# Performance work log

Measured on AMD Instinct MI355X. Metric: run time of the kernel, lower is better.

The kernel has to match this reference:

```python
import jax, jax.numpy as jnp
import numpy as np

B, N1, N2, K, D, C_IN = 2, 8192, 8192, 16, 64, 131
MLP = [128, 128]
WN_HID = [8, 8]


def _sqdist(src, dst):
    # src [B,N,3], dst [B,M,3] -> [B,N,M], clamped at 0 like the torch code
    d = (jnp.sum(src * src, -1)[:, :, None]
         + jnp.sum(dst * dst, -1)[:, None, :]
         - 2.0 * jnp.einsum('bnc,bmc->bnm', src, dst))
    return jnp.maximum(d, 0.0)


def _knn(k, xyz, query):
    # k smallest distances (torch.topk largest=False)
    _, idx = jax.lax.top_k(-_sqdist(query, xyz), k)
    return idx  # [B,S,k]


def _gather(points, idx):
    # points [B,N,C], idx [B,S,K] -> [B,S,K,C]
    return jax.vmap(lambda p, i: p[i])(points, idx)


def _mlp(x, Ws, bs, act):
    # x [B,N,K,Cin]; 1x1 Conv2d == per-point linear
    for W, b in zip(Ws, bs):
        x = act(jnp.einsum('bnkc,oc->bnko', x, W) + b)
    return x


_leaky = lambda x: jax.nn.leaky_relu(x, 0.1)
_relu = jax.nn.relu


def setup_inputs() -> dict:
    key = jax.random.key(0)
    ks = iter(jax.random.split(key, 32))

    def conv(cout, cin):
        s = 1.0 / np.sqrt(cin)
        w = jax.random.uniform(next(ks), (cout, cin), jnp.float32, -s, s)
        b = jax.random.uniform(next(ks), (cout,), jnp.float32, -s, s)
        return w, b

    inp = {
        'pc1': jax.random.normal(next(ks), (B, 3, N1), jnp.float32),
        'pc2': jax.random.normal(next(ks), (B, 3, N2), jnp.float32),
        'feature1': jax.random.normal(next(ks), (B, D, N1), jnp.float32),
        'feature2': jax.random.normal(next(ks), (B, D, N2), jnp.float32),
    }
    # main mlp convs: 131 -> 128 -> 128
    c = C_IN
    for i, co in enumerate(MLP):
        inp[f'mlp_W{i}'], inp[f'mlp_b{i}'] = conv(co, c)
        c = co
    # weightnet1/2: 3 -> 8 -> 8 -> 128
    for name in ('wn1', 'wn2'):
        dims = [3] + WN_HID + [MLP[-1]]
        for i in range(len(dims) - 1):
            inp[f'{name}_W{i}'], inp[f'{name}_b{i}'] = conv(dims[i + 1], dims[i])
    return inp


def reference(pc1, pc2, feature1, feature2,
              mlp_W0, mlp_b0, mlp_W1, mlp_b1,
              wn1_W0, wn1_b0, wn1_W1, wn1_b1, wn1_W2, wn1_b2,
              wn2_W0, wn2_b0, wn2_W1, wn2_b1, wn2_W2, wn2_b2):
    nsample = K
    p1 = pc1.transpose(0, 2, 1)    # [B,N1,3]
    p2 = pc2.transpose(0, 2, 1)    # [B,N2,3]
    f1 = feature1.transpose(0, 2, 1)  # [B,N1,D1]
    f2 = feature2.transpose(0, 2, 1)  # [B,N2,D2]
    b, n1, _ = p1.shape

    # cross-cloud KNN grouping
    idx = _knn(nsample, p2, p1)                 # [B,N1,K]
    direction_xyz = _gather(p2, idx) - p1[:, :, None, :]   # [B,N1,K,3]
    gf2 = _gather(f2, idx)                      # [B,N1,K,D2]
    gf1 = jnp.broadcast_to(f1[:, :, None, :], (b, n1, nsample, f1.shape[-1]))
    new_features = jnp.concatenate([gf1, gf2, direction_xyz], -1)  # [B,N1,K,131]

    new_features = _mlp(new_features, [mlp_W0, mlp_W1], [mlp_b0, mlp_b1], _leaky)
    weights = _mlp(direction_xyz, [wn1_W0, wn1_W1, wn1_W2],
                   [wn1_b0, wn1_b1, wn1_b2], _relu)
    new_features = jnp.sum(weights * new_features, axis=2)  # [B,N1,Cout]

    # self KNN re-aggregation
    idx2 = _knn(nsample, p1, p1)
    dir2 = _gather(p1, idx2) - p1[:, :, None, :]
    weights2 = _mlp(dir2, [wn2_W0, wn2_W1, wn2_W2],
                    [wn2_b0, wn2_b1, wn2_b2], _relu)
    grouped = _gather(new_features, idx2)        # [B,N1,K,Cout]
    out = jnp.sum(weights2 * grouped, axis=2)    # [B,N1,Cout]
    return out.transpose(0, 2, 1)                # [B,Cout,N1]
```

## Files before the change

kernel.cpp:

```cpp
#include <hip/hip_runtime.h>

typedef __attribute__((ext_vector_type(8))) short short8;
typedef __attribute__((ext_vector_type(4))) float f32x4;

#define NPTS 8192
#define NB 2
#define KNN 16
#define KP 20
#define CAP 128
#define LDX 168
#define LDH 136

__device__ inline ushort f2bf(float x){
  unsigned u = __float_as_uint(x);
  return (ushort)((u + 0x7FFFu + ((u >> 16) & 1u)) >> 16);
}
__device__ inline float leaky(float x){ return x > 0.f ? x : 0.1f * x; }
__device__ inline f32x4 mfma16(short8 a, short8 b, f32x4 c){
  return __builtin_amdgcn_mfma_f32_16x16x32_bf16(a, b, c, 0, 0, 0);
}
__device__ inline int cellkey(float x, float y, float z){
  int ix = (int)((x + 3.f) * (16.f / 6.f));
  int iy = (int)((y + 3.f) * (16.f / 6.f));
  int iz = (int)((z + 3.f) * (16.f / 6.f));
  ix = ix < 0 ? 0 : (ix > 15 ? 15 : ix);
  iy = iy < 0 ? 0 : (iy > 15 ? 15 : iy);
  iz = iz < 0 ? 0 : (iz > 15 ? 15 : iz);
  int key = 0;
  #pragma unroll
  for (int i = 0; i < 4; ++i)
    key |= (((ix >> i) & 1) << (3 * i + 2)) | (((iy >> i) & 1) << (3 * i + 1)) | (((iz >> i) & 1) << (3 * i));
  return key;
}

__global__ __launch_bounds__(256) void k_misc(const float* __restrict__ pc1, const float* __restrict__ pc2,
                                              float4* __restrict__ p1, float4* __restrict__ p2,
                                              const float* __restrict__ W0, const float* __restrict__ W1,
                                              ushort* __restrict__ W0p, ushort* __restrict__ W1p){
  int bid = blockIdx.x;
  if (bid < 64){
    int i = bid * 256 + threadIdx.x;
    int b = i >> 13, n = i & (NPTS - 1);
    const float* s1 = pc1 + (size_t)b * 3 * NPTS + n;
    const float* s2 = pc2 + (size_t)b * 3 * NPTS + n;
    p1[i] = make_float4(s1[0], s1[NPTS], s1[2 * NPTS], 0.f);
    p2[i] = make_float4(s2[0], s2[NPTS], s2[2 * NPTS], 0.f);
  } else if (bid == 64){
    for (int e = threadIdx.x; e < 8 * 5 * 64 * 8; e += 256){
      int i = e & 7, ln = (e >> 3) & 63, t = e >> 9, kt = t % 5, ct = t / 5;
      int col = ct * 16 + (ln & 15), k = kt * 32 + 8 * (ln >> 4) + i;
      W0p[e] = f2bf(k < 131 ? W0[col * 131 + k] : 0.f);
    }
  } else {
    for (int e = threadIdx.x; e < 8 * 4 * 64 * 8; e += 256){
      int i = e & 7, ln = (e >> 3) & 63, t = e >> 9, kt = t & 3, ct = t >> 2;
      int col = ct * 16 + (ln & 15), k = kt * 32 + 8 * (ln >> 4) + i;
      W1p[e] = f2bf(W1[col * 128 + k]);
    }
  }
}

__global__ __launch_bounds__(256) void k_transpose(const float* __restrict__ f1, const float* __restrict__ f2,
                                                   ushort* __restrict__ o1, ushort* __restrict__ o2){
  __shared__ ushort tile[64][257];
  int bid = blockIdx.x;
  int feat = bid >> 6; int b = (bid >> 5) & 1; int n0 = (bid & 31) * 256;
  const float* src = (feat ? f2 : f1) + (size_t)b * 64 * NPTS;
  ushort* dst = (feat ? o2 : o1) + (size_t)b * NPTS * 64;
  for (int rep = 0; rep < 64; ++rep){
    int lin = rep * 256 + threadIdx.x;
    int j = lin >> 8, nn = lin & 255;
    tile[j][nn] = f2bf(src[(size_t)j * NPTS + n0 + nn]);
  }
  __syncthreads();
  for (int rep = 0; rep < 64; ++rep){
    int lin = rep * 256 + threadIdx.x;
    int nn = lin >> 6, j = lin & 63;
    dst[(size_t)(n0 + nn) * 64 + j] = tile[j][nn];
  }
}

__global__ __launch_bounds__(1024) void k_sort(const float4* __restrict__ p1, const float4* __restrict__ p2,
                                               float4* __restrict__ sp1, float4* __restrict__ sp2,
                                               int* __restrict__ cs1, int* __restrict__ cs2){
  __shared__ int hist[4096];
  __shared__ int tsum[1024];
  int bid = blockIdx.x;
  int b = bid >> 1, cloud = bid & 1;
  const float4* src = (cloud ? p2 : p1) + b * NPTS;
  float4* dst = (cloud ? sp2 : sp1) + b * NPTS;
  int* cs = (cloud ? cs2 : cs1) + b * 4100;
  int tid = threadIdx.x;
  #pragma unroll
  for (int i = 0; i < 4; ++i) hist[tid + i * 1024] = 0;
  __syncthreads();
  int keys[8];
  #pragma unroll
  for (int i = 0; i < 8; ++i){
    float4 v = src[i * 1024 + tid];
    keys[i] = cellkey(v.x, v.y, v.z);
    atomicAdd(&hist[keys[i]], 1);
  }
  __syncthreads();
  int h[4], s = 0;
  #pragma unroll
  for (int i = 0; i < 4; ++i){ h[i] = hist[tid * 4 + i]; s += h[i]; }
  tsum[tid] = s;
  __syncthreads();
  for (int off = 1; off < 1024; off <<= 1){
    int v = tsum[tid];
    if (tid >= off) v += tsum[tid - off];
    __syncthreads();
    tsum[tid] = v;
    __syncthreads();
  }
  int ex = tid ? tsum[tid - 1] : 0;
  #pragma unroll
  for (int i = 0; i < 4; ++i){ int c = h[i]; hist[tid * 4 + i] = ex; cs[tid * 4 + i] = ex; ex += c; }
  if (tid == 1023) cs[4096] = NPTS;
  __syncthreads();
  #pragma unroll
  for (int i = 0; i < 8; ++i){
    float4 v = src[i * 1024 + tid];
    int pos = atomicAdd(&hist[keys[i]], 1);
    dst[pos] = make_float4(v.x, v.y, v.z, __int_as_float(i * 1024 + tid));
  }
}

__global__ __launch_bounds__(256) void k_knn(const float4* __restrict__ p1,
                                             const float4* __restrict__ sp1, const float4* __restrict__ sp2,
                                             const int* __restrict__ cs1, const int* __restrict__ cs2,
                                             int* __restrict__ idx1, int* __restrict__ idx2){
  __shared__ float sx[1024], sy[1024], sz[1024];
  __shared__ int bufS[4][4][CAP];
  int tid = threadIdx.x, lane = tid & 63, wv = tid >> 6;
  int bid = blockIdx.x;
  int task = bid >> 10, rem = bid & 1023;
  int b = rem >> 9; int q0 = (rem & 511) * 16;
  const float4* __restrict__ cpb = (task ? sp1 : sp2) + b * NPTS;
  const int* __restrict__ cs = (task ? cs1 : cs2) + b * 4100;
  int* __restrict__ outIdx = task ? idx2 : idx1;
  int qbase = b * NPTS + q0 + wv * 4;
  float qx[4], qy[4], qz[4], thr[4]; int cnt[4];
  #pragma unroll
  for (int i = 0; i < 4; ++i){
    float4 qq = p1[qbase + i];
    qx[i] = qq.x; qy[i] = qq.y; qz[i] = qq.z;
  }
  #pragma unroll
  for (int q = 0; q < 4; ++q){
    int key = cellkey(qx[q], qy[q], qz[q]);
    int st = cs[key], en = cs[key + 1];
    int wstart = st + ((en - st) >> 1) - 128;
    wstart = wstart < 0 ? 0 : (wstart > NPTS - 256 ? NPTS - 256 : wstart);
    float dw[4];
    #pragma unroll
    for (int i = 0; i < 4; ++i){
      float4 c = cpb[wstart + i * 64 + lane];
      float dx = c.x - qx[q], dy = c.y - qy[q], dz = c.z - qz[q];
      dw[i] = fmaf(dx, dx, fmaf(dy, dy, dz * dz));
    }
    float mn = fminf(fminf(dw[0], dw[1]), fminf(dw[2], dw[3]));
    float mx = mn;
    #pragma unroll
    for (int off = 1; off < 64; off <<= 1) mx = fmaxf(mx, __shfl_xor(mx, off));
    float lo = 0.f, hi = __uint_as_float(__float_as_uint(mx) + 1u);
    #pragma unroll
    for (int it = 0; it < 16; ++it){
      float mid = 0.5f * (lo + hi);
      int c = __popcll(__ballot(dw[0] < mid)) + __popcll(__ballot(dw[1] < mid))
            + __popcll(__ballot(dw[2] < mid)) + __popcll(__ballot(dw[3] < mid));
      if (c >= KP) hi = mid; else lo = mid;
    }
    thr[q] = __uint_as_float(__float_as_uint(hi) + 1u);
    cnt[q] = 0;
  }
  for (int ch = 0; ch < 8; ++ch){
    __syncthreads();
    for (int t = tid; t < 1024; t += 256){
      float4 cc = cpb[ch * 1024 + t];
      sx[t] = cc.x; sy[t] = cc.y; sz[t] = cc.z;
    }
    __syncthreads();
    for (int it = 0; it < 16; ++it){
      float cx = sx[it * 64 + lane], cy = sy[it * 64 + lane], cz = sz[it * 64 + lane];
      int jb = ch * 1024 + it * 64;
      #pragma unroll
      for (int q = 0; q < 4; ++q){
        float dx = cx - qx[q], dy = cy - qy[q], dz = cz - qz[q];
        float d = fmaf(dx, dx, fmaf(dy, dy, dz * dz));
        bool pass = d < thr[q];
        unsigned long long m = __ballot(pass);
        if (m){
          int pre = __popcll(m & ((1ull << lane) - 1ull));
          int pos = cnt[q] + pre;
          if (pass && pos < CAP) bufS[wv][q][pos] = jb + lane;
          cnt[q] += __popcll(m);
        }
      }
    }
  }
  #pragma unroll 1
  for (int q = 0; q < 4; ++q){
    size_t orow = (size_t)(b * NPTS + q0 + wv * 4 + q) * KNN;
    int T = cnt[q];
    if (T <= CAP){
      double d0 = 1e300, d1 = 1e300; int o0 = 0, o1 = 0, s0 = 0x7fffffff, s1 = 0x7fffffff;
      if (lane < T){
        s0 = bufS[wv][q][lane];
        float4 c = cpb[s0];
        o0 = __float_as_int(c.w);
        double dx = (double)c.x - (double)qx[q];
        double dy = (double)c.y - (double)qy[q];
        double dz = (double)c.z - (double)qz[q];
        d0 = dx * dx + dy * dy + dz * dz;
      }
      if (lane + 64 < T){
        s1 = bufS[wv][q][lane + 64];
        float4 c = cpb[s1];
        o1 = __float_as_int(c.w);
        double dx = (double)c.x - (double)qx[q];
        double dy = (double)c.y - (double)qy[q];
        double dz = (double)c.z - (double)qz[q];
        d1 = dx * dx + dy * dy + dz * dz;
      }
      int r0 = 0, r1 = 0;
      #pragma unroll 4
      for (int j = 0; j < T; ++j){
        int sj = bufS[wv][q][j];
        float4 c = cpb[sj];
        double dx = (double)c.x - (double)qx[q];
        double dy = (double)c.y - (double)qy[q];
        double dz = (double)c.z - (double)qz[q];
        double dj = dx * dx + dy * dy + dz * dz;
        if (dj < d0 || (dj == d0 && sj < s0)) ++r0;
        if (dj < d1 || (dj == d1 && sj < s1)) ++r1;
      }
      if (lane < T && r0 < KNN) outIdx[orow + r0] = o0;
      if (lane + 64 < T && r1 < KNN) outIdx[orow + r1] = o1;
    } else {
      float sdq = 1e30f; int siq = 0; float th = thr[q];
      for (int t = lane; t < NPTS; t += 64){
        int base0 = t - lane;
        float4 c = cpb[t];
        float dx = c.x - qx[q], dy = c.y - qy[q], dz = c.z - qz[q];
        float d = fmaf(dx, dx, fmaf(dy, dy, dz * dz));
        unsigned long long m = __ballot(d < th);
        while (m){
          int src = __ffsll((unsigned long long)m) - 1;
          m &= m - 1;
          float dv = __shfl(d, src);
          if (dv >= th) continue;
          int iv = base0 + src;
          float ud = __shfl_up(sdq, 1);
          int   ui = __shfl_up(siq, 1);
          int pos = __popcll(__ballot(sdq <= dv) & 0xFFFFFull);
          bool lt = lane < pos;
          bool eq = lane == pos;
          float nd = lt ? sdq : (eq ? dv : ud);
          int   ni = lt ? siq : (eq ? iv : ui);
          sdq = nd; siq = ni;
          th = fminf(th, __shfl(nd, KP - 1));
        }
      }
      double dd = -1.0; int orig = 0;
      if (lane < KP){
        float4 cc = cpb[siq];
        orig = __float_as_int(cc.w);
        double dx = (double)cc.x - (double)qx[q];
        double dy = (double)cc.y - (double)qy[q];
        double dz = (double)cc.z - (double)qz[q];
        dd = dx * dx + dy * dy + dz * dz;
      }
      #pragma unroll
      for (int rep = 0; rep < 4; ++rep){
        double mx = dd; int mi = lane;
        #pragma unroll
        for (int off = 32; off; off >>= 1){
          double om = __shfl_xor(mx, off);
          int oi = __shfl_xor(mi, off);
          if (om > mx || (om == mx && oi < mi)){ mx = om; mi = oi; }
        }
        if (lane == mi) dd = -1.0;
      }
      unsigned long long keep = __ballot(dd >= 0.0);
      int rank = __popcll(keep & ((1ull << lane) - 1ull));
      if (dd >= 0.0) outIdx[orow + rank] = orig;
    }
  }
}

__global__ __launch_bounds__(256) void k_fused(
    const float4* __restrict__ p1, const float4* __restrict__ p2,
    const ushort* __restrict__ f1b, const ushort* __restrict__ f2b,
    const int* __restrict__ idx1,
    const ushort* __restrict__ W0p, const ushort* __restrict__ W1p,
    const float* __restrict__ b0, const float* __restrict__ b1,
    const float* __restrict__ wn1W0, const float* __restrict__ wn1b0,
    const float* __restrict__ wn1W1, const float* __restrict__ wn1b1,
    const float* __restrict__ wn1W2, const float* __restrict__ wn1b2,
    float* __restrict__ NF)
{
  __shared__ ushort Xs[128 * LDX];
  __shared__ float dirS[128][4];
  __shared__ float h2S[128][8];
  __shared__ float W2s[128][8];
  __shared__ float b0S[128], b1S[128], b2S[128];
  __shared__ int idxS[128];
  int tid = threadIdx.x, lane = tid & 63, wv = tid >> 6;
  int bid = blockIdx.x;
  int b = bid >> 10; int n0 = (bid & 1023) << 3;
  int base = b * NPTS;
  for (int t = tid; t < 1024; t += 256) ((float*)W2s)[t] = wn1W2[t];
  if (tid < 128){
    b0S[tid] = b0[tid]; b1S[tid] = b1[tid]; b2S[tid] = wn1b2[tid];
    int p = tid >> 4;
    int id = idx1[(size_t)(base + n0 + p) * KNN + (tid & 15)];
    idxS[tid] = id;
    float4 c = p2[base + id];
    float4 q = p1[base + n0 + p];
    float dx = c.x - q.x, dy = c.y - q.y, dz = c.z - q.z;
    dirS[tid][0] = dx; dirS[tid][1] = dy; dirS[tid][2] = dz; dirS[tid][3] = 0.f;
    ushort* xr = Xs + tid * LDX;
    xr[128] = f2bf(dx); xr[129] = f2bf(dy); xr[130] = f2bf(dz);
    #pragma unroll
    for (int j = 131; j < 160; ++j) xr[j] = 0;
  }
  __syncthreads();
  {
    int r = tid >> 1, hf = tid & 1;
    const uint4* s = (const uint4*)(hf ? (f2b + (size_t)(base + idxS[r]) * 64)
                                       : (f1b + (size_t)(base + n0 + (r >> 4)) * 64));
    uint4* d = (uint4*)(Xs + r * LDX + hf * 64);
    #pragma unroll
    for (int j = 0; j < 8; ++j) d[j] = s[j];
  }
  __syncthreads();
  int r0 = wv * 32;
  f32x4 zero4 = {0.f, 0.f, 0.f, 0.f};
  f32x4 acc[2][8];
  #pragma unroll
  for (int mt = 0; mt < 2; ++mt)
    #pragma unroll
    for (int ct = 0; ct < 8; ++ct) acc[mt][ct] = zero4;
  #pragma unroll
  for (int kt = 0; kt < 5; ++kt){
    const ushort* ab = Xs + (r0 + (lane & 15)) * LDX + kt * 32 + 8 * (lane >> 4);
    short8 a0 = *(const short8*)ab;
    short8 a1 = *(const short8*)(ab + 16 * LDX);
    #pragma unroll
    for (int ct = 0; ct < 8; ++ct){
      short8 bb = *(const short8*)(W0p + (size_t)((ct * 5 + kt) * 64 + lane) * 8);
      acc[0][ct] = mfma16(a0, bb, acc[0][ct]);
      acc[1][ct] = mfma16(a1, bb, acc[1][ct]);
    }
  }
  __syncthreads();
  ushort* Hs = Xs;
  #pragma unroll
  for (int mt = 0; mt < 2; ++mt)
    #pragma unroll
    for (int ct = 0; ct < 8; ++ct){
      int col = ct * 16 + (lane & 15);
      float bb = b0S[col];
      #pragma unroll
      for (int r = 0; r < 4; ++r){
        int row = r0 + mt * 16 + 4 * (lane >> 4) + r;
        Hs[row * LDH + col] = f2bf(leaky(acc[mt][ct][r] + bb));
      }
    }
  if (tid < 128){
    float d0 = dirS[tid][0], d1 = dirS[tid][1], d2 = dirS[tid][2];
    float h1[8];
    #pragma unroll
    for (int i = 0; i < 8; ++i)
      h1[i] = fmaxf(fmaf(wn1W0[i * 3 + 2], d2, fmaf(wn1W0[i * 3 + 1], d1, fmaf(wn1W0[i * 3], d0, wn1b0[i]))), 0.f);
    #pragma unroll
    for (int i = 0; i < 8; ++i){
      float s = wn1b1[i];
      #pragma unroll
      for (int j = 0; j < 8; ++j) s = fmaf(wn1W1[i * 8 + j], h1[j], s);
      h2S[tid][i] = fmaxf(s, 0.f);
    }
  }
  __syncthreads();
  #pragma unroll
  for (int mt = 0; mt < 2; ++mt)
    #pragma unroll
    for (int ct = 0; ct < 8; ++ct) acc[mt][ct] = zero4;
  #pragma unroll
  for (int kt = 0; kt < 4; ++kt){
    const ushort* ab = Hs + (r0 + (lane & 15)) * LDH + kt * 32 + 8 * (lane >> 4);
    short8 a0 = *(const short8*)ab;
    short8 a1 = *(const short8*)(ab + 16 * LDH);
    #pragma unroll
    for (int ct = 0; ct < 8; ++ct){
      short8 bb = *(const short8*)(W1p + (size_t)((ct * 4 + kt) * 64 + lane) * 8);
      acc[0][ct] = mfma16(a0, bb, acc[0][ct]);
      acc[1][ct] = mfma16(a1, bb, acc[1][ct]);
    }
  }
  #pragma unroll
  for (int ct = 0; ct < 8; ++ct){
    int col = ct * 16 + (lane & 15);
    float4 w2a = *(const float4*)&W2s[col][0];
    float4 w2b = *(const float4*)&W2s[col][4];
    float bw = b2S[col], bg = b1S[col];
    #pragma unroll
    for (int mt = 0; mt < 2; ++mt){
      float s = 0.f;
      #pragma unroll
      for (int r = 0; r < 4; ++r){
        int row = r0 + mt * 16 + 4 * (lane >> 4) + r;
        const float4 ha = *(const float4*)&h2S[row][0];
        const float4 hb = *(const float4*)&h2S[row][4];
        float w = bw;
        w = fmaf(w2a.x, ha.x, w); w = fmaf(w2a.y, ha.y, w); w = fmaf(w2a.z, ha.z, w); w = fmaf(w2a.w, ha.w, w);
        w = fmaf(w2b.x, hb.x, w); w = fmaf(w2b.y, hb.y, w); w = fmaf(w2b.z, hb.z, w); w = fmaf(w2b.w, hb.w, w);
        w = fmaxf(w, 0.f);
        float g = leaky(acc[mt][ct][r] + bg);
        s = fmaf(w, g, s);
      }
      s += __shfl_xor(s, 16);
      s += __shfl_xor(s, 32);
      if (lane < 16) NF[(size_t)(base + n0 + wv * 2 + mt) * 128 + col] = s;
    }
  }
}

__global__ __launch_bounds__(256) void k_reagg(
    const float4* __restrict__ p1, const int* __restrict__ idx2,
    const float* __restrict__ NF,
    const float* __restrict__ wn2W0, const float* __restrict__ wn2b0,
    const float* __restrict__ wn2W1, const float* __restrict__ wn2b1,
    const float* __restrict__ wn2W2, const float* __restrict__ wn2b2,
    float* __restrict__ out)
{
  __shared__ float h2L[4][16][8];
  __shared__ int idxL[4][16];
  __shared__ float outT[128][20];
  int tid = threadIdx.x, lane = tid & 63, wv = tid >> 6;
  int bid = blockIdx.x;
  int b = bid >> 9; int n0 = (bid & 511) * 16;
  int base = b * NPTS;
  for (int pp = 0; pp < 4; ++pp){
    int np = wv * 4 + pp;
    int n = n0 + np;
    if (lane < 16){
      int id = idx2[(size_t)(base + n) * KNN + lane];
      idxL[wv][lane] = id;
      float4 c = p1[base + id];
      float4 q = p1[base + n];
      float d0 = c.x - q.x, d1 = c.y - q.y, d2 = c.z - q.z;
      float h1[8];
      #pragma unroll
      for (int i = 0; i < 8; ++i)
        h1[i] = fmaxf(fmaf(wn2W0[i * 3 + 2], d2, fmaf(wn2W0[i * 3 + 1], d1, fmaf(wn2W0[i * 3], d0, wn2b0[i]))), 0.f);
      #pragma unroll
      for (int i = 0; i < 8; ++i){
        float s = wn2b1[i];
        #pragma unroll
        for (int j = 0; j < 8; ++j) s = fmaf(wn2W1[i * 8 + j], h1[j], s);
        h2L[wv][lane][i] = fmaxf(s, 0.f);
      }
    }
    __syncthreads();
    #pragma unroll
    for (int hf = 0; hf < 2; ++hf){
      int c = hf * 64 + lane;
      float4 w2a = *(const float4*)(wn2W2 + c * 8);
      float4 w2b = *(const float4*)(wn2W2 + c * 8 + 4);
      float accv = 0.f, bw = wn2b2[c];
      #pragma unroll
      for (int k = 0; k < 16; ++k){
        const float4 ha = *(const float4*)&h2L[wv][k][0];
        const float4 hb = *(const float4*)&h2L[wv][k][4];
        float w = bw;
        w = fmaf(w2a.x, ha.x, w); w = fmaf(w2a.y, ha.y, w); w = fmaf(w2a.z, ha.z, w); w = fmaf(w2a.w, ha.w, w);
        w = fmaf(w2b.x, hb.x, w); w = fmaf(w2b.y, hb.y, w); w = fmaf(w2b.z, hb.z, w); w = fmaf(w2b.w, hb.w, w);
        w = fmaxf(w, 0.f);
        float g = NF[(size_t)(base + idxL[wv][k]) * 128 + c];
        accv = fmaf(w, g, accv);
      }
      outT[c][np] = accv;
    }
    __syncthreads();
  }
  {
    int c = tid >> 1, jh = (tid & 1) * 8;
    float4 v0 = *(const float4*)&outT[c][jh];
    float4 v1 = *(const float4*)&outT[c][jh + 4];
    size_t ob = ((size_t)b * 128 + c) * NPTS + n0 + jh;
    *(float4*)(out + ob) = v0;
    *(float4*)(out + ob + 4) = v1;
  }
}

extern "C" void kernel_launch(void* const* d_in, const int* in_sizes, int n_in,
                              void* d_out, int out_size, void* d_ws, size_t ws_size,
                              hipStream_t stream)
{
  const float* pc1 = (const float*)d_in[0];
  const float* pc2 = (const float*)d_in[1];
  const float* f1  = (const float*)d_in[2];
  const float* f2  = (const float*)d_in[3];
  const float* mW0 = (const float*)d_in[4];
  const float* mb0 = (const float*)d_in[5];
  const float* mW1 = (const float*)d_in[6];
  const float* mb1 = (const float*)d_in[7];
  const float* w1W0 = (const float*)d_in[8];
  const float* w1b0 = (const float*)d_in[9];
  const float* w1W1 = (const float*)d_in[10];
  const float* w1b1 = (const float*)d_in[11];
  const float* w1W2 = (const float*)d_in[12];
  const float* w1b2 = (const float*)d_in[13];
  const float* w2W0 = (const float*)d_in[14];
  const float* w2b0 = (const float*)d_in[15];
  const float* w2W1 = (const float*)d_in[16];
  const float* w2b1 = (const float*)d_in[17];
  const float* w2W2 = (const float*)d_in[18];
  const float* w2b2 = (const float*)d_in[19];

  char* ws = (char*)d_ws;
  float4* p1f4 = (float4*)(ws + 0);
  float4* p2f4 = (float4*)(ws + 262144);
  ushort* f1b  = (ushort*)(ws + 524288);
  ushort* f2b  = (ushort*)(ws + 2621440);
  int* idx1    = (int*)(ws + 4718592);
  int* idx2    = (int*)(ws + 6815744);
  ushort* W0p  = (ushort*)(ws + 8912896);
  ushort* W1p  = (ushort*)(ws + 8953856);
  float* NF    = (float*)(ws + 8986624);
  float4* sp1  = (float4*)(ws + 8986624);
  float4* sp2  = (float4*)(ws + 9248768);
  int* cs1     = (int*)(ws + 9510912);
  int* cs2     = (int*)(ws + 9543712);
  float* out   = (float*)d_out;

  hipLaunchKernelGGL(k_misc, dim3(66), dim3(256), 0, stream, pc1, pc2, p1f4, p2f4, mW0, mW1, W0p, W1p);
  hipLaunchKernelGGL(k_sort, dim3(4), dim3(1024), 0, stream, p1f4, p2f4, sp1, sp2, cs1, cs2);
  hipLaunchKernelGGL(k_transpose, dim3(128), dim3(256), 0, stream, f1, f2, f1b, f2b);
  hipLaunchKernelGGL(k_knn, dim3(2048), dim3(256), 0, stream, p1f4, sp1, sp2, cs1, cs2, idx1, idx2);
  hipLaunchKernelGGL(k_fused, dim3(2048), dim3(256), 0, stream, p1f4, p2f4, f1b, f2b, idx1,
                     W0p, W1p, mb0, mb1, w1W0, w1b0, w1W1, w1b1, w1W2, w1b2, NF);
  hipLaunchKernelGGL(k_reagg, dim3(1024), dim3(256), 0, stream, p1f4, idx2, NF,
                     w2W0, w2b0, w2W1, w2b1, w2W2, w2b2, out);
}
```

Before: 390.3 us.

## Restrict KNN candidate scan to grid cells overlapping the threshold sphere

Replaces the brute-force scan over all 8192 sorted points per query with a walk over the Morton-keyed grid cells that intersect a cube of radius sqrt(threshold) around the query. Points in those cells are read straight from global memory via the cell start table, which removes the shared-memory staging and the block-wide syncs. This cuts distance evaluations sharply but brings per-query divergent loops and uncoalesced, irregular global reads. Correctness depends on the clamped boundary cells covering every candidate under the threshold.

```diff
diff --git a/kernel.cpp b/kernel.cpp
--- a/kernel.cpp
+++ b/kernel.cpp
@@ -31,6 +31,17 @@
   for (int i = 0; i < 4; ++i)
     key |= (((ix >> i) & 1) << (3 * i + 2)) | (((iy >> i) & 1) << (3 * i + 1)) | (((iz >> i) & 1) << (3 * i));
   return key;
+}
+__device__ inline int ikey(int ix, int iy, int iz){
+  int key = 0;
+  #pragma unroll
+  for (int i = 0; i < 4; ++i)
+    key |= (((ix >> i) & 1) << (3 * i + 2)) | (((iy >> i) & 1) << (3 * i + 1)) | (((iz >> i) & 1) << (3 * i));
+  return key;
+}
+__device__ inline int cellc(float v){
+  int i = (int)floorf((v + 3.f) * (16.f / 6.f));
+  return i < 0 ? 0 : (i > 15 ? 15 : i);
 }
 
 __global__ __launch_bounds__(256) void k_misc(const float* __restrict__ pc1, const float* __restrict__ pc2,
@@ -131,7 +142,6 @@
                                              const float4* __restrict__ sp1, const float4* __restrict__ sp2,
                                              const int* __restrict__ cs1, const int* __restrict__ cs2,
                                              int* __restrict__ idx1, int* __restrict__ idx2){
-  __shared__ float sx[1024], sy[1024], sz[1024];
   __shared__ int bufS[4][4][CAP];
   int tid = threadIdx.x, lane = tid & 63, wv = tid >> 6;
   int bid = blockIdx.x;
@@ -175,30 +185,37 @@
     thr[q] = __uint_as_float(__float_as_uint(hi) + 1u);
     cnt[q] = 0;
   }
-  for (int ch = 0; ch < 8; ++ch){
-    __syncthreads();
-    for (int t = tid; t < 1024; t += 256){
-      float4 cc = cpb[ch * 1024 + t];
-      sx[t] = cc.x; sy[t] = cc.y; sz[t] = cc.z;
-    }
-    __syncthreads();
-    for (int it = 0; it < 16; ++it){
-      float cx = sx[it * 64 + lane], cy = sy[it * 64 + lane], cz = sz[it * 64 + lane];
-      int jb = ch * 1024 + it * 64;
-      #pragma unroll
-      for (int q = 0; q < 4; ++q){
-        float dx = cx - qx[q], dy = cy - qy[q], dz = cz - qz[q];
-        float d = fmaf(dx, dx, fmaf(dy, dy, dz * dz));
-        bool pass = d < thr[q];
-        unsigned long long m = __ballot(pass);
-        if (m){
-          int pre = __popcll(m & ((1ull << lane) - 1ull));
-          int pos = cnt[q] + pre;
-          if (pass && pos < CAP) bufS[wv][q][pos] = jb + lane;
-          cnt[q] += __popcll(m);
+  #pragma unroll 1
+  for (int q = 0; q < 4; ++q){
+    float s = sqrtf(thr[q]);
+    int xlo = cellc(qx[q] - s), xhi = cellc(qx[q] + s);
+    int ylo = cellc(qy[q] - s), yhi = cellc(qy[q] + s);
+    int zlo = cellc(qz[q] - s), zhi = cellc(qz[q] + s);
+    int cq = 0;
+    for (int ix = xlo; ix <= xhi; ++ix){
+      for (int iy = ylo; iy <= yhi; ++iy){
+        for (int iz = zlo; iz <= zhi; ++iz){
+          int key = ikey(ix, iy, iz);
+          int st = cs[key], en = cs[key + 1];
+          for (int t0 = st; t0 < en; t0 += 64){
+            int t = t0 + lane;
+            bool pass = false;
+            if (t < en){
+              float4 c = cpb[t];
+              float dx = c.x - qx[q], dy = c.y - qy[q], dz = c.z - qz[q];
+              pass = fmaf(dx, dx, fmaf(dy, dy, dz * dz)) < thr[q];
+            }
+            unsigned long long m = __ballot(pass);
+            if (m){
+              int pre = __popcll(m & ((1ull << lane) - 1ull));
+              if (pass && cq + pre < CAP) bufS[wv][q][cq + pre] = t;
+              cq += __popcll(m);
+            }
+          }
         }
       }
     }
+    cnt[q] = cq;
   }
   #pragma unroll 1
   for (int q = 0; q < 4; ++q){
```

Result: slower. 589.0 us (+50.9%).
